# Kernel tuning notes

Hardware: AMD Instinct MI355X
Metric: run time of the kernel (lower is better)

Reference implementation:

```python
import jax, jax.numpy as jnp
import numpy as np

B, S, CIN, COUT, W, M, P = 32, 8192, 2, 1, 64, 16, 24


def setup_inputs() -> dict:
    key = jax.random.key(0)
    ks = jax.random.split(key, 12)

    def lin(k, o, i):
        return (jax.random.uniform(k, (o, i), jnp.float32) * 2 - 1) / np.float32(np.sqrt(i))

    scale = np.float32(1.0 / (W * W))  # SpectralConv1d init scale 1/(in*out)
    return {
        "x": jax.random.normal(ks[0], (B, S, CIN), jnp.float32),
        "fc0_w": lin(ks[1], W, CIN),
        "fc0_b": jnp.zeros((W,), jnp.float32),
        "conv_wr": jax.random.uniform(ks[2], (4, W, W, M), jnp.float32) * scale,
        "conv_wi": jax.random.uniform(ks[3], (4, W, W, M), jnp.float32) * scale,
        "pw_w": lin(ks[4], 4 * W, W).reshape(4, W, W),  # 1x1 conv weights (out,in)
        "pw_b": jnp.zeros((4, W), jnp.float32),
        "fc1_w": lin(ks[5], 128, W),
        "fc1_b": jnp.zeros((128,), jnp.float32),
        "fc2_w": lin(ks[6], COUT, 128),
        "ica_w": lin(ks[7], P, 128),
        "ica_b": jnp.zeros((P,), jnp.float32),
    }


def spectral_conv(h, wr, wi, n):
    # h: (B, W, S). Keep first M rfft modes, complex-multiply, inverse rfft.
    xf = jnp.fft.rfft(h, axis=-1)[..., :M]          # (B, W, M) complex
    w = wr + 1j * wi                                 # (W, W, M)
    of = jnp.einsum('bix,iox->box', xf, w)           # (B, W, M)
    of = jnp.pad(of, ((0, 0), (0, 0), (0, n // 2 + 1 - M)))
    return jnp.fft.irfft(of, n=n, axis=-1)


def reference(x, fc0_w, fc0_b, conv_wr, conv_wi, pw_w, pw_b, fc1_w, fc1_b, fc2_w, ica_w, ica_b):
    b, s, _ = x.shape
    h = x @ fc0_w.T + fc0_b                          # lift: (B, S, W)
    h = h.transpose(0, 2, 1)                         # (B, W, S)
    for l in range(4):
        x1 = spectral_conv(h, conv_wr[l], conv_wi[l], s)
        x2 = jnp.einsum('oi,bis->bos', pw_w[l], h) + pw_b[l][None, :, None]
        h = x1 + x2
        if l < 3:                                    # no relu after layer 3 (as in torch code)
            h = jax.nn.relu(h)
    h = h.transpose(0, 2, 1)                         # (B, S, W)
    h = h @ fc1_w.T + fc1_b                          # (B, S, 128)
    h_ = jax.nn.relu(h)
    # broadcast ICA decomposition: (B,S,1,128)*(1,1,COUT,128)
    components = h_[:, :, None, :] * fc2_w[None, None, :, :]
    tc = components @ ica_w.T + ica_b                # (B, S, COUT, P)
    out = tc.sum(-1)                                 # (B, S, COUT)
    return out, tc
```

## Files before the change

### kernel.cpp

```cpp
#include <hip/hip_runtime.h>
#include <math.h>

#define SB 8192
#define NB 32
#define WC 64
#define NM 16
#define NKC 32
#define NP 24
#define NSC 16
#define LP 132


__global__ __launch_bounds__(256) void k_table(float* __restrict__ T) {
    int s = blockIdx.x * 256 + threadIdx.x;
    float* row = T + (size_t)s * NKC;
    #pragma unroll
    for (int k = 0; k < NM; ++k) {
        int m = (k * s) & (SB - 1);
        double ang = (double)m * (6.283185307179586476925286766559 / (double)SB);
        row[2 * k]     = (float)cos(ang);
        row[2 * k + 1] = (float)sin(ang);
    }
}

__global__ __launch_bounds__(256) void k_prep(const float* __restrict__ ica_w,
                                              const float* __restrict__ fc2_w,
                                              float* __restrict__ icaT) {
    int tid = blockIdx.x * 256 + threadIdx.x;
    int c = tid / NP;
    int p = tid - c * NP;
    icaT[c * NP + p] = ica_w[p * 128 + c] * fc2_w[c];
}

__global__ __launch_bounds__(256) void k_prepw(const float* __restrict__ pw_w,
                                               float* __restrict__ pwT) {
    int tid = blockIdx.x * 256 + threadIdx.x;
    int l = tid >> 12, k = (tid >> 6) & 63, o = tid & 63;
    pwT[tid] = pw_w[(size_t)l * 4096 + o * 64 + k];
}

__global__ __launch_bounds__(256) void k_lift(const float* __restrict__ x,
                                              const float* __restrict__ fc0_w,
                                              const float* __restrict__ fc0_b,
                                              float* __restrict__ h) {
    int b = blockIdx.y;
    int s = blockIdx.x * 256 + threadIdx.x;
    float2 xv = ((const float2*)x)[(size_t)b * SB + s];
    #pragma unroll
    for (int w = 0; w < WC; ++w) {
        float v = fmaf(xv.x, fc0_w[2 * w], fmaf(xv.y, fc0_w[2 * w + 1], fc0_b[w]));
        h[((size_t)(b * WC + w)) * SB + s] = v;
    }
}

__global__ __launch_bounds__(256) void k_dft(const float* __restrict__ h,
                                             const float* __restrict__ T,
                                             float* __restrict__ xfp) {
    __shared__ float hT[64][LP];
    __shared__ float Tt[32][LP];
    int blk = blockIdx.x;
    int b  = blk >> 4;
    int sc = blk & (NSC - 1);
    int t  = threadIdx.x;
    int g = t >> 4, j = t & 15;

    float acc[4][2];
    #pragma unroll
    for (int i = 0; i < 4; ++i) { acc[i][0] = 0.f; acc[i][1] = 0.f; }

    const float* hb = h + (size_t)b * WC * SB;
    int ch   = t >> 2;
    int part = t & 3;
    int sl   = t >> 1;
    int jj0  = (t & 1) * 16;

    for (int st = 0; st < 4; ++st) {
        int s_base = sc * 512 + st * 128;

        const float* hrow = hb + (size_t)ch * SB + s_base;
        #pragma unroll
        for (int r = 0; r < 8; ++r) {
            int so = (part + 4 * r) * 4;
            *(float4*)&hT[ch][so] = *(const float4*)(hrow + so);
        }
        {
            const float4* src = (const float4*)(T + (size_t)(s_base + sl) * NKC + jj0);
            float4 a = src[0], c4 = src[1], d = src[2], e = src[3];
            Tt[jj0 +  0][sl] = a.x;  Tt[jj0 +  1][sl] = a.y;
            Tt[jj0 +  2][sl] = a.z;  Tt[jj0 +  3][sl] = a.w;
            Tt[jj0 +  4][sl] = c4.x; Tt[jj0 +  5][sl] = c4.y;
            Tt[jj0 +  6][sl] = c4.z; Tt[jj0 +  7][sl] = c4.w;
            Tt[jj0 +  8][sl] = d.x;  Tt[jj0 +  9][sl] = d.y;
            Tt[jj0 + 10][sl] = d.z;  Tt[jj0 + 11][sl] = d.w;
            Tt[jj0 + 12][sl] = e.x;  Tt[jj0 + 13][sl] = e.y;
            Tt[jj0 + 14][sl] = e.z;  Tt[jj0 + 15][sl] = e.w;
        }
        __syncthreads();

        #pragma unroll 4
        for (int step = 0; step < 32; ++step) {
            int s4 = step * 4;
            float4 ta = *(const float4*)&Tt[j][s4];
            float4 tb = *(const float4*)&Tt[j + 16][s4];
            #pragma unroll
            for (int i = 0; i < 4; ++i) {
                float4 hv = *(const float4*)&hT[g * 4 + i][s4];
                acc[i][0] = fmaf(hv.x, ta.x, fmaf(hv.y, ta.y,
                            fmaf(hv.z, ta.z, fmaf(hv.w, ta.w, acc[i][0]))));
                acc[i][1] = fmaf(hv.x, tb.x, fmaf(hv.y, tb.y,
                            fmaf(hv.z, tb.z, fmaf(hv.w, tb.w, acc[i][1]))));
            }
        }
        __syncthreads();
    }

    float* dst = xfp + ((size_t)(sc * NB + b)) * 2048;
    #pragma unroll
    for (int i = 0; i < 4; ++i) {
        dst[(g * 4 + i) * 32 + j]      = acc[i][0];
        dst[(g * 4 + i) * 32 + j + 16] = acc[i][1];
    }
}

__global__ __launch_bounds__(256) void k_red(const float* __restrict__ xfp,
                                             float* __restrict__ xf) {
    int idx = blockIdx.x * 256 + threadIdx.x;
    int b = idx >> 11;
    int r = idx & 2047;
    float s = 0.f;
    #pragma unroll
    for (int sc = 0; sc < NSC; ++sc)
        s += xfp[((size_t)(sc * NB + b)) * 2048 + r];
    xf[idx] = s;
}

__global__ __launch_bounds__(256) void k_mix(const float* __restrict__ xf,
                                             const float* __restrict__ wr,
                                             const float* __restrict__ wi,
                                             float* __restrict__ ofT) {
    int tid = blockIdx.x * 256 + threadIdx.x;
    int k = tid & 15;
    int o = (tid >> 4) & 63;
    int b = tid >> 10;
    float orr = 0.f, oii = 0.f;
    const float2* xfb = (const float2*)(xf + (size_t)b * WC * NKC);
    #pragma unroll 4
    for (int i = 0; i < WC; ++i) {
        float2 cs = xfb[i * NM + k];
        float wrv = wr[(i * WC + o) * NM + k];
        float wiv = wi[(i * WC + o) * NM + k];
        orr = fmaf(cs.x, wrv, fmaf(cs.y, wiv, orr));
        oii = fmaf(cs.x, wiv, fmaf(-cs.y, wrv, oii));
    }
    float alpha = (k == 0 ? 1.f : 2.f) / (float)SB;
    ofT[((size_t)b * NKC + 2 * k) * 64 + o]     = alpha * orr;
    ofT[((size_t)b * NKC + 2 * k + 1) * 64 + o] = -alpha * oii;
}

__global__ __launch_bounds__(256) void k_update(float* __restrict__ h,
                                                const float* __restrict__ T,
                                                const float* __restrict__ ofT,
                                                const float* __restrict__ pwT,
                                                const float* __restrict__ pwb,
                                                int relu) {
    __shared__ float hS[96][68];
    int t = threadIdx.x;
    int b = blockIdx.y;
    int s0 = blockIdx.x * 64;
    int lane_s = t & 63;
    int g = __builtin_amdgcn_readfirstlane((t >> 6) & 3);
    int ob = g * 16;

    {
        int ch = t >> 2, part = t & 3;
        const float* hrow = h + ((size_t)(b * WC + ch)) * SB + s0;
        #pragma unroll
        for (int r = 0; r < 4; ++r) {
            int so = (part + 4 * r) * 4;
            *(float4*)&hS[ch][so] = *(const float4*)(hrow + so);
        }
    }
    {
        int sl = t >> 2, q = t & 3;
        const float4* src = (const float4*)(T + (size_t)(s0 + sl) * NKC + q * 8);
        float4 a = src[0], c4 = src[1];
        hS[64 + q*8 + 0][sl] = a.x;  hS[64 + q*8 + 1][sl] = a.y;
        hS[64 + q*8 + 2][sl] = a.z;  hS[64 + q*8 + 3][sl] = a.w;
        hS[64 + q*8 + 4][sl] = c4.x; hS[64 + q*8 + 5][sl] = c4.y;
        hS[64 + q*8 + 6][sl] = c4.z; hS[64 + q*8 + 7][sl] = c4.w;
    }
    __syncthreads();

    float acc[16];
    #pragma unroll
    for (int o = 0; o < 16; ++o) acc[o] = pwb[ob + o];

    const float* wbase0 = pwT + ob;
    const float* wbase1 = ofT + ((size_t)b * NKC) * 64 + ob;

    for (int kc = 0; kc < 8; ++kc) {
        #pragma unroll
        for (int u = 0; u < 8; ++u) {
            int k = kc * 8 + u;
            float hval = hS[k][lane_s];
            const float* w = wbase0 + k * 64;
            #pragma unroll
            for (int o = 0; o < 16; ++o)
                acc[o] = fmaf(w[o], hval, acc[o]);
        }
    }
    for (int kc = 0; kc < 4; ++kc) {
        #pragma unroll
        for (int u = 0; u < 8; ++u) {
            int j = kc * 8 + u;
            float hval = hS[64 + j][lane_s];
            const float* w = wbase1 + j * 64;
            #pragma unroll
            for (int o = 0; o < 16; ++o)
                acc[o] = fmaf(w[o], hval, acc[o]);
        }
    }

    float* hw = h + (size_t)b * WC * SB + s0 + lane_s;
    #pragma unroll
    for (int o = 0; o < 16; ++o) {
        float v = acc[o];
        if (relu) v = fmaxf(v, 0.f);
        hw[(size_t)(ob + o) * SB] = v;
    }
}

__global__ __launch_bounds__(256) void k_final(const float* __restrict__ h,
                                               const float* __restrict__ fc1_w,
                                               const float* __restrict__ fc1_b,
                                               const float* __restrict__ icaT,
                                               const float* __restrict__ ica_b,
                                               float* __restrict__ out,
                                               float* __restrict__ tc) {
    int b = blockIdx.y;
    int s = blockIdx.x * 256 + threadIdx.x;

    float hv[64];
    const float* hcol = h + (size_t)b * WC * SB + s;
    #pragma unroll
    for (int i = 0; i < 64; ++i) hv[i] = hcol[(size_t)i * SB];

    float acc[NP];
    #pragma unroll
    for (int p = 0; p < NP; ++p) acc[p] = ica_b[p];

    for (int cc = 0; cc < 16; ++cc) {
        float tv8[8];
        #pragma unroll
        for (int u = 0; u < 8; ++u) {
            int c = cc * 8 + u;
            float t = fc1_b[c];
            const float* w = fc1_w + c * WC;
            #pragma unroll
            for (int i = 0; i < 64; ++i) t = fmaf(w[i], hv[i], t);
            tv8[u] = fmaxf(t, 0.f);
        }
        #pragma unroll
        for (int u = 0; u < 8; ++u) {
            const float* e = icaT + (cc * 8 + u) * NP;
            #pragma unroll
            for (int p = 0; p < NP; ++p)
                acc[p] = fmaf(tv8[u], e[p], acc[p]);
        }
    }

    float osum = 0.f;
    #pragma unroll
    for (int p = 0; p < NP; ++p) osum += acc[p];
    size_t idx = (size_t)b * SB + s;
    out[idx] = osum;

    float4* t4 = (float4*)(tc + idx * NP);
    t4[0] = make_float4(acc[0],  acc[1],  acc[2],  acc[3]);
    t4[1] = make_float4(acc[4],  acc[5],  acc[6],  acc[7]);
    t4[2] = make_float4(acc[8],  acc[9],  acc[10], acc[11]);
    t4[3] = make_float4(acc[12], acc[13], acc[14], acc[15]);
    t4[4] = make_float4(acc[16], acc[17], acc[18], acc[19]);
    t4[5] = make_float4(acc[20], acc[21], acc[22], acc[23]);
}

extern "C" void kernel_launch(void* const* d_in, const int* in_sizes, int n_in,
                              void* d_out, int out_size, void* d_ws, size_t ws_size,
                              hipStream_t stream) {
    const float* x     = (const float*)d_in[0];
    const float* fc0_w = (const float*)d_in[1];
    const float* fc0_b = (const float*)d_in[2];
    const float* cwr   = (const float*)d_in[3];
    const float* cwi   = (const float*)d_in[4];
    const float* pw_w  = (const float*)d_in[5];
    const float* pw_b  = (const float*)d_in[6];
    const float* fc1_w = (const float*)d_in[7];
    const float* fc1_b = (const float*)d_in[8];
    const float* fc2_w = (const float*)d_in[9];
    const float* ica_w = (const float*)d_in[10];
    const float* ica_b = (const float*)d_in[11];

    float* out = (float*)d_out;
    float* tc  = out + (size_t)NB * SB;

    float* ws   = (float*)d_ws;
    float* h    = ws;
    float* T    = ws + 16777216;
    float* xf   = ws + 17039360;
    float* ofT  = ws + 17104896;
    float* icaT = ws + 17170432;
    float* pwT  = ws + 17173504;
    float* xfp  = tc;

    k_table<<<32, 256, 0, stream>>>(T);
    k_prep<<<12, 256, 0, stream>>>(ica_w, fc2_w, icaT);
    k_prepw<<<64, 256, 0, stream>>>(pw_w, pwT);
    k_lift<<<dim3(32, 32), 256, 0, stream>>>(x, fc0_w, fc0_b, h);

    for (int l = 0; l < 4; ++l) {
        k_dft<<<NB * NSC, 256, 0, stream>>>(h, T, xfp);
        k_red<<<256, 256, 0, stream>>>(xfp, xf);
        k_mix<<<128, 256, 0, stream>>>(xf, cwr + (size_t)l * WC * WC * NM,
                                       cwi + (size_t)l * WC * WC * NM, ofT);
        k_update<<<dim3(128, 32), 256, 0, stream>>>(h, T, ofT,
                                                    pwT + (size_t)l * 4096,
                                                    pw_b + (size_t)l * WC,
                                                    (l < 3) ? 1 : 0);
    }

    k_final<<<dim3(32, 32), 256, 0, stream>>>(h, fc1_w, fc1_b, icaT, ica_b, out, tc);
}
```

Baseline: 470.4 us.

## Split final MLP hidden channels across waves with LDS staging and reduction

The final kernel now handles 64 sequence positions per block instead of 256. It stages the 64-channel h tile in shared memory and splits the 128 fc1 hidden units across four waves of 32 each. Partial ICA accumulators are reduced through LDS, and the tc output is written with coalesced stores instead of per-thread float4 strided writes. This cuts per-thread register pressure and gives four times more blocks for occupancy, at the cost of extra LDS traffic and synchronisation.

Measured after the change: 465.1 us. About the same (-1.1%).

```diff
diff --git a/kernel.cpp b/kernel.cpp
--- a/kernel.cpp
+++ b/kernel.cpp
@@ -237,51 +237,79 @@
                                                const float* __restrict__ ica_b,
                                                float* __restrict__ out,
                                                float* __restrict__ tc) {
+    __shared__ float u_lds[6144];
+    float (*hS)[68] = (float(*)[68])u_lds;
+    int t = threadIdx.x;
     int b = blockIdx.y;
-    int s = blockIdx.x * 256 + threadIdx.x;
-
-    float hv[64];
-    const float* hcol = h + (size_t)b * WC * SB + s;
-    #pragma unroll
-    for (int i = 0; i < 64; ++i) hv[i] = hcol[(size_t)i * SB];
+    int s0 = blockIdx.x * 64;
+    int lane_s = t & 63;
+    int wv = __builtin_amdgcn_readfirstlane((t >> 6) & 3);
+    int c0 = wv * 32;
+
+    {
+        int ch = t >> 2, part = t & 3;
+        const float* hrow = h + ((size_t)(b * WC + ch)) * SB + s0;
+        #pragma unroll
+        for (int r = 0; r < 4; ++r) {
+            int so = (part + 4 * r) * 4;
+            *(float4*)&hS[ch][so] = *(const float4*)(hrow + so);
+        }
+    }
+    __syncthreads();
 
     float acc[NP];
     #pragma unroll
-    for (int p = 0; p < NP; ++p) acc[p] = ica_b[p];
-
-    for (int cc = 0; cc < 16; ++cc) {
-        float tv8[8];
-        #pragma unroll
-        for (int u = 0; u < 8; ++u) {
-            int c = cc * 8 + u;
-            float t = fc1_b[c];
-            const float* w = fc1_w + c * WC;
-            #pragma unroll
-            for (int i = 0; i < 64; ++i) t = fmaf(w[i], hv[i], t);
-            tv8[u] = fmaxf(t, 0.f);
-        }
-        #pragma unroll
-        for (int u = 0; u < 8; ++u) {
-            const float* e = icaT + (cc * 8 + u) * NP;
-            #pragma unroll
-            for (int p = 0; p < NP; ++p)
-                acc[p] = fmaf(tv8[u], e[p], acc[p]);
-        }
-    }
-
-    float osum = 0.f;
-    #pragma unroll
-    for (int p = 0; p < NP; ++p) osum += acc[p];
-    size_t idx = (size_t)b * SB + s;
-    out[idx] = osum;
-
-    float4* t4 = (float4*)(tc + idx * NP);
-    t4[0] = make_float4(acc[0],  acc[1],  acc[2],  acc[3]);
-    t4[1] = make_float4(acc[4],  acc[5],  acc[6],  acc[7]);
-    t4[2] = make_float4(acc[8],  acc[9],  acc[10], acc[11]);
-    t4[3] = make_float4(acc[12], acc[13], acc[14], acc[15]);
-    t4[4] = make_float4(acc[16], acc[17], acc[18], acc[19]);
-    t4[5] = make_float4(acc[20], acc[21], acc[22], acc[23]);
+    for (int p = 0; p < NP; ++p) acc[p] = 0.f;
+
+    for (int cp = 0; cp < 16; ++cp) {
+        int c = c0 + 2 * cp;
+        float tv0 = fc1_b[c];
+        float tv1 = fc1_b[c + 1];
+        const float* w0 = fc1_w + c * WC;
+        const float* w1 = w0 + WC;
+        for (int ioct = 0; ioct < 8; ++ioct) {
+            float xs[8];
+            #pragma unroll
+            for (int u = 0; u < 8; ++u) xs[u] = hS[ioct * 8 + u][lane_s];
+            #pragma unroll
+            for (int u = 0; u < 8; ++u) {
+                tv0 = fmaf(w0[ioct * 8 + u], xs[u], tv0);
+                tv1 = fmaf(w1[ioct * 8 + u], xs[u], tv1);
+            }
+        }
+        tv0 = fmaxf(tv0, 0.f);
+        tv1 = fmaxf(tv1, 0.f);
+        const float* e0 = icaT + c * NP;
+        const float* e1 = e0 + NP;
+        #pragma unroll
+        for (int p = 0; p < NP; ++p)
+            acc[p] = fmaf(tv0, e0[p], fmaf(tv1, e1[p], acc[p]));
+    }
+
+    __syncthreads();
+    #pragma unroll
+    for (int p = 0; p < NP; ++p)
+        u_lds[((t >> 6) * 64 + lane_s) * NP + p] = acc[p];
+    __syncthreads();
+
+    float* tcb = tc + ((size_t)b * SB + s0) * NP;
+    #pragma unroll
+    for (int r = 0; r < 6; ++r) {
+        int e = t + r * 256;
+        int s = e / NP, p = e - s * NP;
+        float v = u_lds[s * NP + p] + u_lds[(64 + s) * NP + p]
+                + u_lds[(128 + s) * NP + p] + u_lds[(192 + s) * NP + p]
+                + ica_b[p];
+        tcb[e] = v;
+        u_lds[s * NP + p] = v;
+    }
+    __syncthreads();
+    if (t < 64) {
+        float osum = 0.f;
+        #pragma unroll
+        for (int p = 0; p < NP; ++p) osum += u_lds[t * NP + p];
+        out[(size_t)b * SB + s0 + t] = osum;
+    }
 }
 
 extern "C" void kernel_launch(void* const* d_in, const int* in_sizes, int n_in,
@@ -328,5 +356,5 @@
                                                     (l < 3) ? 1 : 0);
     }
 
-    k_final<<<dim3(32, 32), 256, 0, stream>>>(h, fc1_w, fc1_b, icaT, ica_b, out, tc);
-}
+    k_final<<<dim3(128, 32), 256, 0, stream>>>(h, fc1_w, fc1_b, icaT, ica_b, out, tc);
+}
```
